# Performance work log

Measured on AMD Instinct MI355X. Metric: run time of the kernel, lower is better.

Reference implementation:

```python
import jax, jax.numpy as jnp
import numpy as np

N_NODES = 100000
N_EDGES = 1600000
DK = 32
OUT_DIM = 32


def setup_inputs() -> dict:
    key = jax.random.key(0)
    ks = jax.random.split(key, 7)
    X = jax.random.normal(ks[0], (N_NODES, DK), dtype=jnp.float32)
    K = jax.random.normal(ks[1], (N_NODES, DK), dtype=jnp.float32)
    V = jax.random.normal(ks[2], (N_NODES, DK), dtype=jnp.float32)
    # output projection (nn.Dense(out_dim)) params
    W_o = jax.random.normal(ks[3], (DK, OUT_DIM), dtype=jnp.float32) / np.sqrt(DK)
    b_o = jnp.zeros((OUT_DIM,), dtype=jnp.float32)
    # sparsity descriptor td: edge list, dst sorted so segment ops see sorted ids
    src = jax.random.randint(ks[4], (N_EDGES,), 0, N_NODES, dtype=jnp.int32)
    dst = jnp.sort(jax.random.randint(ks[5], (N_EDGES,), 0, N_NODES, dtype=jnp.int32))
    return {"X": X, "K": K, "V": V, "W_o": W_o, "b_o": b_o,
            "src": src, "dst": dst, "num_seg": N_NODES}


def reference(X, K, V, W_o, b_o, src, dst, num_seg):
    dk = X.shape[-1]
    # per-edge attention logits: <Q[dst], K[src]> / dk  -> (E,)
    scores = jnp.einsum('ed,ed->e', jnp.take(X, dst, axis=0),
                        jnp.take(K, src, axis=0)) / dk
    # segment (per-neighborhood) softmax over edges sharing a dst node
    seg_max = jax.ops.segment_max(scores, dst, num_segments=num_seg,
                                  indices_are_sorted=True)
    e = jnp.exp(scores - jnp.take(seg_max, dst))
    denom = jax.ops.segment_sum(e, dst, num_segments=num_seg,
                                indices_are_sorted=True)
    alpha = e / jnp.take(denom, dst)  # (E,)
    # weighted aggregation of values, scattered back to nodes -> (N, dk)
    agg = jax.ops.segment_sum(alpha[:, None] * jnp.take(V, src, axis=0), dst,
                              num_segments=num_seg, indices_are_sorted=True)
    # output projection W_o
    return agg @ W_o + b_o
```

## Files before the change

### kernel.cpp

```cpp
#include <hip/hip_runtime.h>
#include <math.h>

#define DK 32
#define OUT_DIM 32

typedef float    f32x4 __attribute__((ext_vector_type(4)));
typedef _Float16 h2    __attribute__((ext_vector_type(2)));
typedef _Float16 h8    __attribute__((ext_vector_type(8)));

#if __has_builtin(__builtin_amdgcn_fdot2)
#define FDOT2(a, b, c) __builtin_amdgcn_fdot2((a), (b), (c), false)
#else
#define FDOT2(a, b, c) ((c) + (float)(a).x * (float)(b).x + (float)(a).y * (float)(b).y)
#endif

__device__ __forceinline__ h2 as_h2(unsigned u) {
    union { unsigned u; h2 h; } v; v.u = u; return v.h;
}
__device__ __forceinline__ unsigned as_u32(h2 h) {
    union { unsigned u; h2 h; } v; v.h = h; return v.u;
}
__device__ __forceinline__ h2 shfl_xor_h2(h2 v, int m) {
    union { unsigned u; h2 h; } x; x.h = v;
    x.u = (unsigned)__shfl_xor((int)x.u, m);
    return x.h;
}

__global__ void prep_kernel(const int* __restrict__ dst,
                            const float* __restrict__ K,
                            const float* __restrict__ V,
                            int E, int N,
                            int* __restrict__ row_ptr,
                            unsigned* __restrict__ KVH) {
    const int t = blockIdx.x * blockDim.x + threadIdx.x;
    if (t < E) {
        const int cur  = dst[t];
        const int prev = (t == 0) ? -1 : dst[t - 1];
        for (int j = prev + 1; j <= cur; ++j) row_ptr[j] = t;
        if (t == E - 1) {
            for (int j = cur + 1; j <= N; ++j) row_ptr[j] = E;
        }
    }
    if (t < N * DK) {
        const int s = t >> 5;
        const int r = t & 31;
        const int c = r >> 2;
        const int q = r & 3;
        const float* srcp = (q < 2) ? K : V;
        const int d0 = c * 4 + (q & 1) * 2;
        h2 h;
        h.x = (_Float16)srcp[s * DK + d0];
        h.y = (_Float16)srcp[s * DK + d0 + 1];
        KVH[t] = as_u32(h);
    }
}

__global__ void build_row_ptr_kernel(const int* __restrict__ dst, int E, int N,
                                     int* __restrict__ row_ptr) {
    int e = blockIdx.x * blockDim.x + threadIdx.x;
    if (e >= E) return;
    int cur  = dst[e];
    int prev = (e == 0) ? -1 : dst[e - 1];
    for (int j = prev + 1; j <= cur; ++j) row_ptr[j] = e;
    if (e == E - 1) {
        for (int j = cur + 1; j <= N; ++j) row_ptr[j] = E;
    }
}

__global__ __launch_bounds__(256) void gat_fused_kernel(
    const float* __restrict__ X, const uint4* __restrict__ KV,
    const float* __restrict__ Wo, const float* __restrict__ bo,
    const int* __restrict__ src, const int* __restrict__ row_ptr,
    float* __restrict__ out, int N) {

    __shared__ uint4 s_part[16 * 17];

    const int tid  = threadIdx.x;
    const int w    = tid >> 6;
    const int lane = tid & 63;
    const int g    = lane >> 3;
    const int c    = lane & 7;

    const int n_blk = blockIdx.x * 16;
    const int n_w   = n_blk + w * 4;

    const int rpv = row_ptr[min(n_w + min(lane, 4), N)];

    const float4* X4 = (const float4*)X;
    unsigned* part32 = (unsigned*)s_part;
    const float scale = 0.03125f;

    for (int i = 0; i < 4; ++i) {
        const int begin = __builtin_amdgcn_readlane(rpv, i);
        const int end   = __builtin_amdgcn_readlane(rpv, i + 1);
        const int n     = n_w + i;

        float4 q = X4[min(n, N - 1) * 8 + c];
        h2 qh01, qh23;
        qh01.x = (_Float16)(q.x * scale);  qh01.y = (_Float16)(q.y * scale);
        qh23.x = (_Float16)(q.z * scale);  qh23.y = (_Float16)(q.w * scale);

        float l = 0.0f;
        h2 acc01 = (h2)0, acc23 = (h2)0;

        for (int e0 = begin; e0 < end; e0 += 16) {
            const int sa = src[min(e0 + g,     end - 1)];
            const int sb = src[min(e0 + 8 + g, end - 1)];
            const uint4 A = KV[sa * 8 + c];
            const uint4 B = KV[sb * 8 + c];

            float p0 = FDOT2(as_h2(A.y), qh23, FDOT2(as_h2(A.x), qh01, 0.0f));
            float p1 = FDOT2(as_h2(B.y), qh23, FDOT2(as_h2(B.x), qh01, 0.0f));
            p0 += __shfl_xor(p0, 1);  p1 += __shfl_xor(p1, 1);
            p0 += __shfl_xor(p0, 2);  p1 += __shfl_xor(p1, 2);
            p0 += __shfl_xor(p0, 4);  p1 += __shfl_xor(p1, 4);

            const float w0 = (e0 + g     < end) ? __expf(p0) : 0.0f;
            const float w1 = (e0 + 8 + g < end) ? __expf(p1) : 0.0f;
            l += w0 + w1;

            h2 wh0; wh0.x = (_Float16)w0; wh0.y = wh0.x;
            h2 wh1; wh1.x = (_Float16)w1; wh1.y = wh1.x;
            acc01 += wh0 * as_h2(A.z);
            acc23 += wh0 * as_h2(A.w);
            acc01 += wh1 * as_h2(B.z);
            acc23 += wh1 * as_h2(B.w);
        }

        l     += __shfl_xor(l, 8);
        acc01 += shfl_xor_h2(acc01, 8);
        acc23 += shfl_xor_h2(acc23, 8);
        l += __shfl_xor(l, 16);  l += __shfl_xor(l, 32);

        const float inv = (end > begin) ? (1.0f / l) : 0.0f;
        h2 invh; invh.x = (_Float16)inv; invh.y = invh.x;
        acc01 *= invh;
        acc23 *= invh;

        if ((g & 1) == 0) {
            const int p   = g >> 1;
            const int row = w * 4 + i;
            const int off = row * 68 + p * 16 + c * 2;
            part32[off]     = as_u32(acc01);
            part32[off + 1] = as_u32(acc23);
        }
    }

    __syncthreads();

    if (w == 0) {
        const int quad = lane >> 4;
        const int col  = lane & 15;

        union BF { h8 v; _Float16 u[8]; };
        BF bf0, bf1;
#pragma unroll
        for (int j2 = 0; j2 < 8; ++j2) {
            bf0.u[j2] = (_Float16)Wo[(quad * 8 + j2) * OUT_DIM + col];
            bf1.u[j2] = (_Float16)Wo[(quad * 8 + j2) * OUT_DIM + 16 + col];
        }
        const float bias0 = bo[col];
        const float bias1 = bo[16 + col];

        union AF { uint4 u; h8 v; };
        f32x4 C0 = {bias0, bias0, bias0, bias0};
        f32x4 C1 = {bias1, bias1, bias1, bias1};
#pragma unroll
        for (int cc = 0; cc < 4; ++cc) {
            AF a;
            a.u = s_part[col * 17 + cc * 4 + quad];
            C0 = __builtin_amdgcn_mfma_f32_16x16x32_f16(a.v, bf0.v, C0, 0, 0, 0);
            C1 = __builtin_amdgcn_mfma_f32_16x16x32_f16(a.v, bf1.v, C1, 0, 0, 0);
        }
#pragma unroll
        for (int r = 0; r < 4; ++r) {
            const int n = n_blk + quad * 4 + r;
            if (n < N) {
                out[n * OUT_DIM + col]      = C0[r];
                out[n * OUT_DIM + 16 + col] = C1[r];
            }
        }
    }
}

__global__ __launch_bounds__(256) void gat_node_f32_kernel(
    const float* __restrict__ X, const float* __restrict__ Km,
    const float* __restrict__ Vm, const float* __restrict__ Wo,
    const float* __restrict__ bo, const int* __restrict__ src,
    const int* __restrict__ row_ptr, float* __restrict__ out, int N) {
    const int tid  = threadIdx.x;
    const int wave = tid >> 6;
    const int lane = tid & 63;
    const int g    = lane >> 3;
    const int c    = lane & 7;
    const int j    = lane & 31;
    const int half = lane >> 5;
    const int n = blockIdx.x * 4 + wave;
    if (n >= N) return;
    const int begin = row_ptr[n];
    const int end   = row_ptr[n + 1];
    const float4* X4 = (const float4*)X;
    const float4* K4 = (const float4*)Km;
    const float4* V4 = (const float4*)Vm;
    const float4 q4 = X4[n * 8 + c];
    float  l   = 0.0f;
    float4 acc = make_float4(0.0f, 0.0f, 0.0f, 0.0f);
    for (int e0 = begin; e0 < end; e0 += 16) {
        const int  ea = e0 + g;
        const int  eb = ea + 8;
        const bool va = ea < end;
        const bool vb = eb < end;
        const int sa = src[min(ea, end - 1)];
        const int sb = src[min(eb, end - 1)];
        const float4 ka  = K4[sa * 8 + c];
        const float4 kb  = K4[sb * 8 + c];
        const float4 vva = V4[sa * 8 + c];
        const float4 vvb = V4[sb * 8 + c];
        float pa = fmaf(ka.x, q4.x, fmaf(ka.y, q4.y, fmaf(ka.z, q4.z, ka.w * q4.w)));
        float pb = fmaf(kb.x, q4.x, fmaf(kb.y, q4.y, fmaf(kb.z, q4.z, kb.w * q4.w)));
        pa += __shfl_xor(pa, 1);  pb += __shfl_xor(pb, 1);
        pa += __shfl_xor(pa, 2);  pb += __shfl_xor(pb, 2);
        pa += __shfl_xor(pa, 4);  pb += __shfl_xor(pb, 4);
        const float wa = va ? __expf(pa * 0.03125f) : 0.0f;
        const float wb = vb ? __expf(pb * 0.03125f) : 0.0f;
        l += wa + wb;
        acc.x = fmaf(wa, vva.x, acc.x);  acc.y = fmaf(wa, vva.y, acc.y);
        acc.z = fmaf(wa, vva.z, acc.z);  acc.w = fmaf(wa, vva.w, acc.w);
        acc.x = fmaf(wb, vvb.x, acc.x);  acc.y = fmaf(wb, vvb.y, acc.y);
        acc.z = fmaf(wb, vvb.z, acc.z);  acc.w = fmaf(wb, vvb.w, acc.w);
    }
#pragma unroll
    for (int m = 8; m <= 32; m <<= 1) {
        l     += __shfl_xor(l, m);
        acc.x += __shfl_xor(acc.x, m);
        acc.y += __shfl_xor(acc.y, m);
        acc.z += __shfl_xor(acc.z, m);
        acc.w += __shfl_xor(acc.w, m);
    }
    const float inv = (end > begin) ? (1.0f / l) : 0.0f;
    float ag[4] = {acc.x, acc.y, acc.z, acc.w};
    float s = 0.0f;
#pragma unroll
    for (int k = 0; k < 32; ++k) {
        const float a = __int_as_float(
            __builtin_amdgcn_readlane(__float_as_int(ag[k & 3]), k >> 2));
        s = fmaf(a, Wo[k * OUT_DIM + j], s);
    }
    if (half == 0) {
        out[n * OUT_DIM + j] = fmaf(s, inv, bo[j]);
    }
}

extern "C" void kernel_launch(void* const* d_in, const int* in_sizes, int n_in,
                              void* d_out, int out_size, void* d_ws, size_t ws_size,
                              hipStream_t stream) {
    const float* X  = (const float*)d_in[0];
    const float* Km = (const float*)d_in[1];
    const float* Vm = (const float*)d_in[2];
    const float* Wo = (const float*)d_in[3];
    const float* bo = (const float*)d_in[4];
    const int* src  = (const int*)d_in[5];
    const int* dst  = (const int*)d_in[6];

    const int N = in_sizes[0] / DK;
    const int E = in_sizes[5];

    int* row_ptr = (int*)d_ws;
    const size_t kv_off = (((size_t)(N + 1) * 4) + 127) & ~(size_t)127;
    unsigned* KV = (unsigned*)((char*)d_ws + kv_off);
    const size_t need = kv_off + (size_t)N * DK * 4;
    float* out = (float*)d_out;

    const int tb = 256;

    if (ws_size >= need) {
        const int total  = N * DK;
        const int prep_n = (E > total) ? E : total;
        prep_kernel<<<(prep_n + tb - 1) / tb, tb, 0, stream>>>(dst, Km, Vm, E, N,
                                                               row_ptr, KV);
        const int grid = (N + 15) / 16;
        gat_fused_kernel<<<grid, 256, 0, stream>>>(X, (const uint4*)KV, Wo, bo,
                                                   src, row_ptr, out, N);
    } else {
        build_row_ptr_kernel<<<(E + tb - 1) / tb, tb, 0, stream>>>(dst, E, N, row_ptr);
        const int grid = (N + 3) / 4;
        gat_node_f32_kernel<<<grid, 256, 0, stream>>>(X, Km, Vm, Wo, bo,
                                                      src, row_ptr, out, N);
    }
}
```

Measured before the change: 143.2 us.

## Interleave edge loops of four nodes per wave to overlap gathers

Result: no change. 143.1 us (-0.1%).

```diff
diff --git a/kernel.cpp b/kernel.cpp
--- a/kernel.cpp
+++ b/kernel.cpp
@@ -90,59 +90,84 @@
     unsigned* part32 = (unsigned*)s_part;
     const float scale = 0.03125f;
 
+    int eb[5];
+#pragma unroll
+    for (int i = 0; i < 5; ++i) eb[i] = __builtin_amdgcn_readlane(rpv, i);
+
+    int   e[4], cap[4];
+    float l[4];
+    h2    q01[4], q23[4], a01[4], a23[4];
+#pragma unroll
     for (int i = 0; i < 4; ++i) {
-        const int begin = __builtin_amdgcn_readlane(rpv, i);
-        const int end   = __builtin_amdgcn_readlane(rpv, i + 1);
-        const int n     = n_w + i;
-
-        float4 q = X4[min(n, N - 1) * 8 + c];
-        h2 qh01, qh23;
-        qh01.x = (_Float16)(q.x * scale);  qh01.y = (_Float16)(q.y * scale);
-        qh23.x = (_Float16)(q.z * scale);  qh23.y = (_Float16)(q.w * scale);
-
-        float l = 0.0f;
-        h2 acc01 = (h2)0, acc23 = (h2)0;
-
-        for (int e0 = begin; e0 < end; e0 += 16) {
-            const int sa = src[min(e0 + g,     end - 1)];
-            const int sb = src[min(e0 + 8 + g, end - 1)];
-            const uint4 A = KV[sa * 8 + c];
-            const uint4 B = KV[sb * 8 + c];
-
-            float p0 = FDOT2(as_h2(A.y), qh23, FDOT2(as_h2(A.x), qh01, 0.0f));
-            float p1 = FDOT2(as_h2(B.y), qh23, FDOT2(as_h2(B.x), qh01, 0.0f));
-            p0 += __shfl_xor(p0, 1);  p1 += __shfl_xor(p1, 1);
-            p0 += __shfl_xor(p0, 2);  p1 += __shfl_xor(p1, 2);
-            p0 += __shfl_xor(p0, 4);  p1 += __shfl_xor(p1, 4);
-
-            const float w0 = (e0 + g     < end) ? __expf(p0) : 0.0f;
-            const float w1 = (e0 + 8 + g < end) ? __expf(p1) : 0.0f;
-            l += w0 + w1;
-
+        e[i]   = eb[i];
+        cap[i] = max(eb[i + 1] - 1, 0);
+        l[i]   = 0.0f;
+        a01[i] = (h2)0;  a23[i] = (h2)0;
+        const float4 q = X4[min(n_w + i, N - 1) * 8 + c];
+        q01[i].x = (_Float16)(q.x * scale);  q01[i].y = (_Float16)(q.y * scale);
+        q23[i].x = (_Float16)(q.z * scale);  q23[i].y = (_Float16)(q.w * scale);
+    }
+
+    while (e[0] < eb[1] || e[1] < eb[2] || e[2] < eb[3] || e[3] < eb[4]) {
+        int s0[4], s1[4];
+#pragma unroll
+        for (int i = 0; i < 4; ++i) {
+            s0[i] = src[min(e[i] + g,     cap[i])];
+            s1[i] = src[min(e[i] + 8 + g, cap[i])];
+        }
+        uint4 A[4], B[4];
+#pragma unroll
+        for (int i = 0; i < 4; ++i) {
+            A[i] = KV[s0[i] * 8 + c];
+            B[i] = KV[s1[i] * 8 + c];
+        }
+
+        float p0[4], p1[4];
+#pragma unroll
+        for (int i = 0; i < 4; ++i) {
+            p0[i] = FDOT2(as_h2(A[i].y), q23[i], FDOT2(as_h2(A[i].x), q01[i], 0.0f));
+            p1[i] = FDOT2(as_h2(B[i].y), q23[i], FDOT2(as_h2(B[i].x), q01[i], 0.0f));
+        }
+#pragma unroll
+        for (int m = 1; m <= 4; m <<= 1) {
+#pragma unroll
+            for (int i = 0; i < 4; ++i) {
+                p0[i] += __shfl_xor(p0[i], m);
+                p1[i] += __shfl_xor(p1[i], m);
+            }
+        }
+#pragma unroll
+        for (int i = 0; i < 4; ++i) {
+            const int end_i = eb[i + 1];
+            const float w0 = (e[i] + g     < end_i) ? __expf(p0[i]) : 0.0f;
+            const float w1 = (e[i] + 8 + g < end_i) ? __expf(p1[i]) : 0.0f;
+            l[i] += w0 + w1;
             h2 wh0; wh0.x = (_Float16)w0; wh0.y = wh0.x;
             h2 wh1; wh1.x = (_Float16)w1; wh1.y = wh1.x;
-            acc01 += wh0 * as_h2(A.z);
-            acc23 += wh0 * as_h2(A.w);
-            acc01 += wh1 * as_h2(B.z);
-            acc23 += wh1 * as_h2(B.w);
-        }
-
-        l     += __shfl_xor(l, 8);
-        acc01 += shfl_xor_h2(acc01, 8);
-        acc23 += shfl_xor_h2(acc23, 8);
-        l += __shfl_xor(l, 16);  l += __shfl_xor(l, 32);
-
-        const float inv = (end > begin) ? (1.0f / l) : 0.0f;
-        h2 invh; invh.x = (_Float16)inv; invh.y = invh.x;
-        acc01 *= invh;
-        acc23 *= invh;
+            a01[i] += wh0 * as_h2(A[i].z);  a23[i] += wh0 * as_h2(A[i].w);
+            a01[i] += wh1 * as_h2(B[i].z);  a23[i] += wh1 * as_h2(B[i].w);
+            e[i] += 16;
+        }
+    }
+
+#pragma unroll
+    for (int i = 0; i < 4; ++i) {
+        l[i]   += __shfl_xor(l[i], 8);
+        a01[i] += shfl_xor_h2(a01[i], 8);
+        a23[i] += shfl_xor_h2(a23[i], 8);
+        l[i] += __shfl_xor(l[i], 16);  l[i] += __shfl_xor(l[i], 32);
+
+        const float inv = (eb[i + 1] > eb[i]) ? (1.0f / l[i]) : 0.0f;
+        h2 iv; iv.x = (_Float16)inv; iv.y = iv.x;
+        a01[i] *= iv;
+        a23[i] *= iv;
 
         if ((g & 1) == 0) {
             const int p   = g >> 1;
             const int row = w * 4 + i;
             const int off = row * 68 + p * 16 + c * 2;
-            part32[off]     = as_u32(acc01);
-            part32[off + 1] = as_u32(acc23);
+            part32[off]     = as_u32(a01[i]);
+            part32[off + 1] = as_u32(a23[i]);
         }
     }
 
```
